# Kernel optimization log

Hardware: AMD Instinct MI355X
Metric: run time of the kernel (lower is better)

## Reference

```python
import jax, jax.numpy as jnp
import numpy as np

def setup_inputs() -> dict:
    key = jax.random.key(0)
    ks = jax.random.split(key, 8)
    b, n, dim = 2, 2048, 512
    h, d, K, M = 8, 64, 32, 131072
    x = jax.random.normal(ks[0], (b, n, dim), dtype=jnp.float32)
    mem_db = jax.random.normal(ks[1], (b, M, 2, d), dtype=jnp.float32)
    knn_idx = jax.random.randint(ks[2], (b, h, n, K), 0, M)
    mem_mask = jax.random.randint(ks[3], (b, h, n, K), 0, 2).astype(bool)
    Wq = jax.random.normal(ks[4], (h * d, dim), dtype=jnp.float32) * 0.02
    Wkv = jax.random.normal(ks[5], (2 * d, dim), dtype=jnp.float32) * 0.02
    Wout = jax.random.normal(ks[6], (dim, h * d), dtype=jnp.float32) * 0.02
    scale_param = jnp.ones((h, 1, 1), dtype=jnp.float32) * np.log(20.0)
    return {"x": x, "mem_db": mem_db, "knn_idx": knn_idx, "mem_mask": mem_mask,
            "Wq": Wq, "Wkv": Wkv, "Wout": Wout, "scale_param": scale_param}

def reference(x, mem_db, knn_idx, mem_mask, Wq, Wkv, Wout, scale_param):
    b, n, dim = x.shape
    h = scale_param.shape[0]
    d = Wq.shape[0] // h
    # projections
    q = jnp.einsum('bnc,ec->bne', x, Wq).reshape(b, n, h, d).transpose(0, 2, 1, 3)  # b h n d
    q = q / jnp.linalg.norm(q, axis=-1, keepdims=True).clip(1e-12)  # l2norm
    kv = jnp.einsum('bnc,ec->bne', x, Wkv)  # [b,n,2d]; detached + added to memory (side effect only)
    scale = jnp.exp(scale_param)  # [h,1,1]
    # per-query KNN gather: mem_db [b,M,2,d], knn_idx [b,h,n,K] -> [b,h,n,K,2,d]
    mem_kv = jax.vmap(lambda db, ix: db[ix])(mem_db, knn_idx)
    mem_k = mem_kv[..., 0, :]  # b h n K d
    mem_v = mem_kv[..., 1, :]
    sim = jnp.einsum('bhid,bhijd->bhij', q, mem_k) * scale  # b h n K
    mask_value = -jnp.finfo(sim.dtype).max
    sim = jnp.where(mem_mask, sim, mask_value)
    attn = jax.nn.softmax(sim, axis=-1)  # stable softmax
    out = jnp.einsum('bhij,bhijd->bhid', attn, mem_v)  # b h n d
    out = out.transpose(0, 2, 1, 3).reshape(b, n, h * d)
    return jnp.einsum('bne,ce->bnc', out, Wout)
```

## Files before the change

kernel.cpp:

```cpp
#include <hip/hip_runtime.h>
#include <hip/hip_bf16.h>
#include <math.h>

#define B_SZ 2
#define N_SEQ 2048
#define DIM 512
#define H_HEADS 8
#define D_HEAD 64
#define K_NN 32
#define M_DB 131072

typedef __attribute__((ext_vector_type(8))) short bf16x8;
typedef __attribute__((ext_vector_type(4))) float f32x4;

#define GLL16(g, l)                                                       \
    __builtin_amdgcn_global_load_lds(                                     \
        (const __attribute__((address_space(1))) unsigned int*)(g),       \
        (__attribute__((address_space(3))) unsigned int*)(l), 16, 0, 0)

__device__ __forceinline__ void cvt_hi_lo(float f, short& h, short& l) {
    unsigned u = __float_as_uint(f);
    unsigned uh = u + (0x7fffu + ((u >> 16) & 1u));
    h = (short)(uh >> 16);
    float r = f - __uint_as_float((uh >> 16) << 16);
    unsigned ur = __float_as_uint(r);
    l = (short)((ur + (0x7fffu + ((ur >> 16) & 1u))) >> 16);
}

__device__ __forceinline__ void split4(float4 a, ushort4& h, ushort4& l) {
    short hh, ll;
    cvt_hi_lo(a.x, hh, ll); h.x = hh; l.x = ll;
    cvt_hi_lo(a.y, hh, ll); h.y = hh; l.y = ll;
    cvt_hi_lo(a.z, hh, ll); h.z = hh; l.z = ll;
    cvt_hi_lo(a.w, hh, ll); h.w = hh; l.w = ll;
}

__global__ __launch_bounds__(256) void prep_kernel(
    const float4* __restrict__ x, const float4* __restrict__ wq,
    const float4* __restrict__ wout,
    ushort4* __restrict__ xhi, ushort4* __restrict__ xlo,
    ushort4* __restrict__ qhi, ushort4* __restrict__ qlo,
    ushort4* __restrict__ ohi, ushort4* __restrict__ olo,
    const unsigned char* __restrict__ mb, int* __restrict__ flag)
{
    const int bid = blockIdx.x;
    const int t = threadIdx.x;
    if (bid < 2048) {
        int i = bid * 256 + t;
        ushort4 h, l;
        split4(x[i], h, l);
        xhi[i] = h; xlo[i] = l;
    } else if (bid < 2560) {
        int i = (bid - 2048) * 256 + t;
        const int n4 = DIM * DIM / 4;
        const float4* src = (i < n4) ? wq : wout;
        ushort4* dh = (i < n4) ? qhi : ohi;
        ushort4* dl = (i < n4) ? qlo : olo;
        int j = (i < n4) ? i : i - n4;
        ushort4 h, l;
        split4(src[j], h, l);
        dh[j] = h; dl[j] = l;
    } else {
        if (t < 64) {
            unsigned char v = 0;
            for (int e = t; e < 1024; e += 64) {
                v |= mb[4 * e + 1];
                v |= mb[4 * e + 2];
                v |= mb[4 * e + 3];
            }
            unsigned long long any = __ballot(v != 0);
            if (t == 0) *flag = (any != 0ull) ? 1 : 0;
        }
    }
}

__global__ __launch_bounds__(256) void gemm_mfma_lds(
    const unsigned short* __restrict__ Ahi, const unsigned short* __restrict__ Alo,
    const unsigned short* __restrict__ Bhi, const unsigned short* __restrict__ Blo,
    float* __restrict__ C, int Mdim, int Ndim, int Kdim)
{
    __shared__ char lds[2][32768];
    const int t = threadIdx.x;
    const int w = t >> 6, lane = t & 63;
    const int r = lane & 15, qd = lane >> 4;
    const int wm = w & 1, wn = w >> 1;
    const int m0 = blockIdx.x * 64;
    const int n0 = blockIdx.y * 64;

    const unsigned short* gsrc[8];
#pragma unroll
    for (int j = 0; j < 8; ++j) {
        const int cl = j * 4 + w;
        const int isB = cl >> 4;
        const int c = cl & 15;
        const int p = c >> 3, s = (c >> 2) & 1, h = c & 3;
        const int row = (isB ? n0 : m0) + 16 * h + r;
        const int col = 32 * s + 8 * qd;
        const unsigned short* plane =
            isB ? (p ? Blo : Bhi) : (p ? Alo : Ahi);
        gsrc[j] = plane + (size_t)row * Kdim + col;
    }

    f32x4 acc[2][2];
#pragma unroll
    for (int i = 0; i < 2; ++i)
#pragma unroll
        for (int j = 0; j < 2; ++j) acc[i][j] = (f32x4){0.f, 0.f, 0.f, 0.f};

    auto stage = [&](int buf, int kstep) {
#pragma unroll
        for (int j = 0; j < 8; ++j) {
            const int cl = j * 4 + w;
            GLL16(gsrc[j] + kstep * 64, &lds[buf][cl * 1024]);
        }
    };

    auto compute = [&](int buf) {
        const char* base = lds[buf];
        bf16x8 A8[2][2][2], B8[2][2][2];
#pragma unroll
        for (int p = 0; p < 2; ++p)
#pragma unroll
            for (int s = 0; s < 2; ++s)
#pragma unroll
                for (int i = 0; i < 2; ++i) {
                    A8[p][s][i] = *(const bf16x8*)(
                        base + ((p * 2 + s) * 4 + 2 * wm + i) * 1024 + lane * 16);
                    B8[p][s][i] = *(const bf16x8*)(
                        base + 16384 +
                        ((p * 2 + s) * 4 + 2 * wn + i) * 1024 + lane * 16);
                }
#pragma unroll
        for (int s = 0; s < 2; ++s)
#pragma unroll
            for (int mi = 0; mi < 2; ++mi)
#pragma unroll
                for (int ni = 0; ni < 2; ++ni) {
                    acc[mi][ni] = __builtin_amdgcn_mfma_f32_16x16x32_bf16(
                        A8[0][s][mi], B8[0][s][ni], acc[mi][ni], 0, 0, 0);
                    acc[mi][ni] = __builtin_amdgcn_mfma_f32_16x16x32_bf16(
                        A8[0][s][mi], B8[1][s][ni], acc[mi][ni], 0, 0, 0);
                    acc[mi][ni] = __builtin_amdgcn_mfma_f32_16x16x32_bf16(
                        A8[1][s][mi], B8[0][s][ni], acc[mi][ni], 0, 0, 0);
                }
    };

    const int nsteps = Kdim >> 6;
    stage(0, 0);
    asm volatile("s_waitcnt vmcnt(0)" ::: "memory");
    __syncthreads();
    for (int ks = 0; ks < nsteps - 1; ++ks) {
        stage((ks + 1) & 1, ks + 1);
        compute(ks & 1);
        asm volatile("s_waitcnt vmcnt(0)" ::: "memory");
        __syncthreads();
    }
    compute((nsteps - 1) & 1);

#pragma unroll
    for (int mi = 0; mi < 2; ++mi)
#pragma unroll
        for (int ni = 0; ni < 2; ++ni)
#pragma unroll
            for (int rr = 0; rr < 4; ++rr)
                C[(size_t)(m0 + 32 * wm + 16 * mi + qd * 4 + rr) * Ndim +
                  n0 + 32 * wn + 16 * ni + r] = acc[mi][ni][rr];
}

__global__ __launch_bounds__(256) void attn_kernel(
    const float* __restrict__ qbuf,
    const float* __restrict__ mem_db,
    const int* __restrict__ knn_idx,
    const void* __restrict__ mem_mask,
    const float* __restrict__ scale_param,
    const int* __restrict__ flag,
    unsigned short* __restrict__ out_hi,
    unsigned short* __restrict__ out_lo)
{
    const int wave = blockIdx.x * 4 + (threadIdx.x >> 6);
    const int lane = threadIdx.x & 63;
    const int sub = lane & 15, grp = lane >> 4;
    const int i = wave % N_SEQ;
    const int bh = wave / N_SEQ;
    const int hi = bh % H_HEADS;
    const int bi = bh / H_HEADS;

    const int bytelayout = *flag;

    const float* qrow = qbuf + (size_t)(bi * N_SEQ + i) * DIM + hi * D_HEAD;
    float qv = qrow[lane];
    float ss = qv * qv;
#pragma unroll
    for (int s = 32; s; s >>= 1) ss += __shfl_xor(ss, s);
    qv = qv / fmaxf(sqrtf(ss), 1e-12f);

    float q4[4];
#pragma unroll
    for (int c = 0; c < 4; ++c) q4[c] = __shfl(qv, 4 * sub + c);

    const float scale = __expf(scale_param[hi]);

    const size_t kb = ((size_t)(bi * H_HEADS + hi) * N_SEQ + i) * K_NN;
    int idxv = 0, maskv = 0;
    if (lane < K_NN) {
        idxv = knn_idx[kb + lane];
        if (bytelayout)
            maskv = ((const unsigned char*)mem_mask)[kb + lane] ? 1 : 0;
        else
            maskv = ((const int*)mem_mask)[kb + lane] ? 1 : 0;
    }

    unsigned long long mbits = __ballot(maskv != 0);
    const bool allmasked = (mbits == 0ull);

    const float* dbb = mem_db + (size_t)bi * M_DB * (2 * D_HEAD);

    float4 kk[8], vv[8];
#pragma unroll
    for (int g = 0; g < 8; ++g) {
        int idx = __shfl(idxv, 4 * g + grp);
        bool mrow = (mbits >> (4 * g + grp)) & 1ull;
        size_t koff = mrow ? (size_t)idx * (2 * D_HEAD) : 0;
        size_t voff = (mrow || allmasked) ? (size_t)idx * (2 * D_HEAD) : 0;
        kk[g] = *(const float4*)(dbb + koff + 4 * sub);
        vv[g] = *(const float4*)(dbb + voff + D_HEAD + 4 * sub);
    }

    float s8[8];
#pragma unroll
    for (int g = 0; g < 8; ++g) {
        float p = q4[0] * kk[g].x + q4[1] * kk[g].y + q4[2] * kk[g].z + q4[3] * kk[g].w;
        p += __shfl_xor(p, 1);
        p += __shfl_xor(p, 2);
        p += __shfl_xor(p, 4);
        p += __shfl_xor(p, 8);
        s8[g] = p;
    }

    float simlane = -INFINITY;
#pragma unroll
    for (int g = 0; g < 8; ++g) {
        float tv = __shfl(s8[g], (lane & 3) << 4);
        if ((lane >> 2) == g) simlane = tv;
    }
    if (lane < K_NN)
        simlane = maskv ? simlane * scale : -3.402823466e38f;

    float m = simlane;
#pragma unroll
    for (int s = 32; s; s >>= 1) m = fmaxf(m, __shfl_xor(m, s));
    float w = __expf(simlane - m);
    float l = w;
#pragma unroll
    for (int s = 32; s; s >>= 1) l += __shfl_xor(l, s);
    float winv = w / l;

    float4 o = {0.f, 0.f, 0.f, 0.f};
#pragma unroll
    for (int g = 0; g < 8; ++g) {
        float wg = __shfl(winv, 4 * g + grp);
        o.x = fmaf(wg, vv[g].x, o.x);
        o.y = fmaf(wg, vv[g].y, o.y);
        o.z = fmaf(wg, vv[g].z, o.z);
        o.w = fmaf(wg, vv[g].w, o.w);
    }
#pragma unroll
    for (int s = 16; s <= 32; s <<= 1) {
        o.x += __shfl_xor(o.x, s);
        o.y += __shfl_xor(o.y, s);
        o.z += __shfl_xor(o.z, s);
        o.w += __shfl_xor(o.w, s);
    }
    if (grp == 0) {
        ushort4 h, l4;
        split4(o, h, l4);
        size_t off = ((size_t)(bi * N_SEQ + i) * DIM + hi * D_HEAD + 4 * sub) >> 2;
        ((ushort4*)out_hi)[off] = h;
        ((ushort4*)out_lo)[off] = l4;
    }
}

extern "C" void kernel_launch(void* const* d_in, const int* in_sizes, int n_in,
                              void* d_out, int out_size, void* d_ws, size_t ws_size,
                              hipStream_t stream) {
    const float* x        = (const float*)d_in[0];
    const float* mem_db   = (const float*)d_in[1];
    const int*   knn_idx  = (const int*)d_in[2];
    const void*  mem_mask = d_in[3];
    const float* Wq       = (const float*)d_in[4];
    const float* Wout     = (const float*)d_in[6];
    const float* scale_p  = (const float*)d_in[7];
    float* out = (float*)d_out;

    const int Mrows = B_SZ * N_SEQ;
    const int n_x   = Mrows * DIM;
    const int n_w   = DIM * DIM;

    char* ws = (char*)d_ws;
    int* flag = (int*)ws;
    float* qbuf = (float*)(ws + 256);
    unsigned short* x_hi  = (unsigned short*)(qbuf + (size_t)n_x);
    unsigned short* x_lo  = x_hi + n_x;
    unsigned short* ao_hi = x_lo + n_x;
    unsigned short* ao_lo = ao_hi + n_x;
    unsigned short* wq_hi = ao_lo + n_x;
    unsigned short* wq_lo = wq_hi + n_w;
    unsigned short* wo_hi = wq_lo + n_w;
    unsigned short* wo_lo = wo_hi + n_w;

    prep_kernel<<<2561, 256, 0, stream>>>(
        (const float4*)x, (const float4*)Wq, (const float4*)Wout,
        (ushort4*)x_hi, (ushort4*)x_lo,
        (ushort4*)wq_hi, (ushort4*)wq_lo, (ushort4*)wo_hi, (ushort4*)wo_lo,
        (const unsigned char*)mem_mask, flag);

    dim3 ggrid(Mrows / 64, DIM / 64);
    gemm_mfma_lds<<<ggrid, 256, 0, stream>>>(x_hi, x_lo, wq_hi, wq_lo, qbuf,
                                             Mrows, DIM, DIM);

    const int n_waves = B_SZ * H_HEADS * N_SEQ;
    attn_kernel<<<n_waves / 4, 256, 0, stream>>>(qbuf, mem_db, knn_idx, mem_mask,
                                                 scale_p, flag, ao_hi, ao_lo);

    gemm_mfma_lds<<<ggrid, 256, 0, stream>>>(ao_hi, ao_lo, wo_hi, wo_lo, out,
                                             Mrows, DIM, DIM);
}
```

Before: 262.9 us.

## Triple-buffer GEMM LDS pipeline with smaller K-step and hoist index loads in attention

The GEMM K-step is halved to 32 and its LDS staging goes from two buffers to three. The loop now waits on vmcnt(4) rather than vmcnt(0), so two stages of global-to-LDS loads stay in flight while the current buffer is computed, and the full __syncthreads is replaced by a raw s_barrier. Separately, the attention kernel issues the knn index and mask loads before the query normalisation, to overlap that latency with the q load and reduction. The smaller K-step doubles the number of loop iterations and barriers, and the vmcnt-based ordering depends on exactly four loads per stage.

```diff
diff --git a/kernel.cpp b/kernel.cpp
--- a/kernel.cpp
+++ b/kernel.cpp
@@ -79,7 +79,7 @@
     const unsigned short* __restrict__ Bhi, const unsigned short* __restrict__ Blo,
     float* __restrict__ C, int Mdim, int Ndim, int Kdim)
 {
-    __shared__ char lds[2][32768];
+    __shared__ char lds[3][16384];
     const int t = threadIdx.x;
     const int w = t >> 6, lane = t & 63;
     const int r = lane & 15, qd = lane >> 4;
@@ -87,18 +87,17 @@
     const int m0 = blockIdx.x * 64;
     const int n0 = blockIdx.y * 64;
 
-    const unsigned short* gsrc[8];
-#pragma unroll
-    for (int j = 0; j < 8; ++j) {
+    const unsigned short* gsrc[4];
+#pragma unroll
+    for (int j = 0; j < 4; ++j) {
         const int cl = j * 4 + w;
-        const int isB = cl >> 4;
-        const int c = cl & 15;
-        const int p = c >> 3, s = (c >> 2) & 1, h = c & 3;
+        const int isB = cl >> 3;
+        const int c = cl & 7;
+        const int p = c >> 2, h = c & 3;
         const int row = (isB ? n0 : m0) + 16 * h + r;
-        const int col = 32 * s + 8 * qd;
         const unsigned short* plane =
             isB ? (p ? Blo : Bhi) : (p ? Alo : Ahi);
-        gsrc[j] = plane + (size_t)row * Kdim + col;
+        gsrc[j] = plane + (size_t)row * Kdim + 8 * qd;
     }
 
     f32x4 acc[2][2];
@@ -109,53 +108,54 @@
 
     auto stage = [&](int buf, int kstep) {
 #pragma unroll
-        for (int j = 0; j < 8; ++j) {
+        for (int j = 0; j < 4; ++j) {
             const int cl = j * 4 + w;
-            GLL16(gsrc[j] + kstep * 64, &lds[buf][cl * 1024]);
+            GLL16(gsrc[j] + kstep * 32, &lds[buf][cl * 1024]);
         }
     };
 
     auto compute = [&](int buf) {
         const char* base = lds[buf];
-        bf16x8 A8[2][2][2], B8[2][2][2];
+        bf16x8 A8[2][2], B8[2][2];
 #pragma unroll
         for (int p = 0; p < 2; ++p)
 #pragma unroll
-            for (int s = 0; s < 2; ++s)
-#pragma unroll
-                for (int i = 0; i < 2; ++i) {
-                    A8[p][s][i] = *(const bf16x8*)(
-                        base + ((p * 2 + s) * 4 + 2 * wm + i) * 1024 + lane * 16);
-                    B8[p][s][i] = *(const bf16x8*)(
-                        base + 16384 +
-                        ((p * 2 + s) * 4 + 2 * wn + i) * 1024 + lane * 16);
-                }
-#pragma unroll
-        for (int s = 0; s < 2; ++s)
-#pragma unroll
-            for (int mi = 0; mi < 2; ++mi)
-#pragma unroll
-                for (int ni = 0; ni < 2; ++ni) {
-                    acc[mi][ni] = __builtin_amdgcn_mfma_f32_16x16x32_bf16(
-                        A8[0][s][mi], B8[0][s][ni], acc[mi][ni], 0, 0, 0);
-                    acc[mi][ni] = __builtin_amdgcn_mfma_f32_16x16x32_bf16(
-                        A8[0][s][mi], B8[1][s][ni], acc[mi][ni], 0, 0, 0);
-                    acc[mi][ni] = __builtin_amdgcn_mfma_f32_16x16x32_bf16(
-                        A8[1][s][mi], B8[0][s][ni], acc[mi][ni], 0, 0, 0);
-                }
+            for (int i = 0; i < 2; ++i) {
+                A8[p][i] = *(const bf16x8*)(
+                    base + (p * 4 + 2 * wm + i) * 1024 + lane * 16);
+                B8[p][i] = *(const bf16x8*)(
+                    base + 8192 + (p * 4 + 2 * wn + i) * 1024 + lane * 16);
+            }
+#pragma unroll
+        for (int mi = 0; mi < 2; ++mi)
+#pragma unroll
+            for (int ni = 0; ni < 2; ++ni) {
+                acc[mi][ni] = __builtin_amdgcn_mfma_f32_16x16x32_bf16(
+                    A8[0][mi], B8[0][ni], acc[mi][ni], 0, 0, 0);
+                acc[mi][ni] = __builtin_amdgcn_mfma_f32_16x16x32_bf16(
+                    A8[0][mi], B8[1][ni], acc[mi][ni], 0, 0, 0);
+                acc[mi][ni] = __builtin_amdgcn_mfma_f32_16x16x32_bf16(
+                    A8[1][mi], B8[0][ni], acc[mi][ni], 0, 0, 0);
+            }
     };
 
-    const int nsteps = Kdim >> 6;
+    const int nsteps = Kdim >> 5;
     stage(0, 0);
+    stage(1, 1);
+    int bc = 0;
+    for (int ks = 0; ks < nsteps - 1; ++ks) {
+        asm volatile("s_waitcnt vmcnt(4)" ::: "memory");
+        __builtin_amdgcn_s_barrier();
+        if (ks + 2 < nsteps) {
+            int bs = bc + 2; if (bs >= 3) bs -= 3;
+            stage(bs, ks + 2);
+        }
+        compute(bc);
+        if (++bc == 3) bc = 0;
+    }
     asm volatile("s_waitcnt vmcnt(0)" ::: "memory");
-    __syncthreads();
-    for (int ks = 0; ks < nsteps - 1; ++ks) {
-        stage((ks + 1) & 1, ks + 1);
-        compute(ks & 1);
-        asm volatile("s_waitcnt vmcnt(0)" ::: "memory");
-        __syncthreads();
-    }
-    compute((nsteps - 1) & 1);
+    __builtin_amdgcn_s_barrier();
+    compute(bc);
 
 #pragma unroll
     for (int mi = 0; mi < 2; ++mi)
@@ -187,19 +187,6 @@
 
     const int bytelayout = *flag;
 
-    const float* qrow = qbuf + (size_t)(bi * N_SEQ + i) * DIM + hi * D_HEAD;
-    float qv = qrow[lane];
-    float ss = qv * qv;
-#pragma unroll
-    for (int s = 32; s; s >>= 1) ss += __shfl_xor(ss, s);
-    qv = qv / fmaxf(sqrtf(ss), 1e-12f);
-
-    float q4[4];
-#pragma unroll
-    for (int c = 0; c < 4; ++c) q4[c] = __shfl(qv, 4 * sub + c);
-
-    const float scale = __expf(scale_param[hi]);
-
     const size_t kb = ((size_t)(bi * H_HEADS + hi) * N_SEQ + i) * K_NN;
     int idxv = 0, maskv = 0;
     if (lane < K_NN) {
@@ -209,6 +196,19 @@
         else
             maskv = ((const int*)mem_mask)[kb + lane] ? 1 : 0;
     }
+
+    const float* qrow = qbuf + (size_t)(bi * N_SEQ + i) * DIM + hi * D_HEAD;
+    float qv = qrow[lane];
+    float ss = qv * qv;
+#pragma unroll
+    for (int s = 32; s; s >>= 1) ss += __shfl_xor(ss, s);
+    qv = qv / fmaxf(sqrtf(ss), 1e-12f);
+
+    float q4[4];
+#pragma unroll
+    for (int c = 0; c < 4; ++c) q4[c] = __shfl(qv, 4 * sub + c);
+
+    const float scale = __expf(scale_param[hi]);
 
     unsigned long long mbits = __ballot(maskv != 0);
     const bool allmasked = (mbits == 0ull);
```

Result: no change. 261.1 us (-0.7%).
